# Optimization experiments

Measured on AMD Instinct MI355X. Metric: run time of the kernel, lower is better.

## Reference

```python
import jax, jax.numpy as jnp
import numpy as np

EMB = 1024
HEAD = 128

def setup_inputs() -> dict:
    key = jax.random.key(0)
    ks = jax.random.split(key, 7)
    B, S = 4, 4096
    x = jax.random.normal(ks[0], (B, S, EMB), dtype=jnp.float32)
    s_in = 1.0 / np.sqrt(EMB)
    Wq = jax.random.uniform(ks[1], (EMB, HEAD), jnp.float32, -s_in, s_in)
    bq = jax.random.uniform(ks[2], (HEAD,), jnp.float32, -s_in, s_in)
    Wk = jax.random.uniform(ks[3], (EMB, HEAD), jnp.float32, -s_in, s_in)
    bk = jax.random.uniform(ks[4], (HEAD,), jnp.float32, -s_in, s_in)
    Wv = jax.random.uniform(ks[5], (EMB, HEAD), jnp.float32, -s_in, s_in)
    bv = jax.random.uniform(ks[6], (HEAD,), jnp.float32, -s_in, s_in)
    return {"decoder_sequence": x, "Wq": Wq, "bq": bq, "Wk": Wk, "bk": bk, "Wv": Wv, "bv": bv}

def reference(decoder_sequence, Wq, bq, Wk, bk, Wv, bv):
    # QKV projections: [B,S,E] @ [E,H] -> [B,S,H]
    Q = decoder_sequence @ Wq + bq
    K = decoder_sequence @ Wk + bk
    V = decoder_sequence @ Wv + bv
    S = decoder_sequence.shape[1]
    scale = 1.0 / jnp.sqrt(jnp.asarray(HEAD, Q.dtype))
    # scores [B,S,S]
    A = jnp.einsum('bid,bjd->bij', Q, K) * scale
    causal = jnp.tril(jnp.ones((S, S), dtype=bool))  # keep lower-triangular incl. diag
    A = jnp.where(causal, A, -jnp.inf)
    A = jax.nn.softmax(A, axis=-1)
    return jnp.einsum('bij,bjd->bid', A, V)
```

## Files before the change

### kernel.cpp

```cpp
#include <hip/hip_runtime.h>
#include <hip/hip_bf16.h>
#include <math.h>

#define S_LEN 4096
#define EMB   1024
#define HEAD  128

typedef short bf16x8 __attribute__((ext_vector_type(8)));
typedef short s16x4  __attribute__((ext_vector_type(4)));
typedef float f32x4  __attribute__((ext_vector_type(4)));
typedef unsigned u32x2 __attribute__((ext_vector_type(2)));
typedef unsigned u32x4 __attribute__((ext_vector_type(4)));

static __device__ __forceinline__ short f2bf(float x){
  unsigned u = __builtin_bit_cast(unsigned, x);
  u += 0x7fffu + ((u >> 16) & 1u);
  return (short)(u >> 16);
}
static __device__ __forceinline__ float bf2f(short s){
  unsigned u = ((unsigned)(unsigned short)s) << 16;
  return __builtin_bit_cast(float, u);
}
static __device__ __forceinline__ unsigned cvtpk(float a, float b){
  unsigned r;
  asm("v_cvt_pk_bf16_f32 %0, %1, %2" : "=v"(r) : "v"(a), "v"(b));
  return r;
}
static __device__ __forceinline__ f32x4 mfma16(bf16x8 a, bf16x8 b, f32x4 c){
  return __builtin_amdgcn_mfma_f32_16x16x32_bf16(a, b, c, 0, 0, 0);
}
static __device__ __forceinline__ void gload16(const void* g, void* l){
  __builtin_amdgcn_global_load_lds((const __attribute__((address_space(1))) unsigned*)g,
                                   (__attribute__((address_space(3))) unsigned*)l, 16, 0, 0);
}

__global__ void prep_w(const float* __restrict__ Wq, const float* __restrict__ bq,
                       const float* __restrict__ Wk, const float* __restrict__ bk,
                       const float* __restrict__ Wv, const float* __restrict__ bv,
                       short* __restrict__ WT, float* __restrict__ bias){
  const float QS = 0.08838834764831845f * 1.4426950408889634f;
  int idx = blockIdx.x * 256 + threadIdx.x;
  int nc  = idx >> 10;
  int k   = idx & 1023;
  int mat = nc >> 7;
  int n   = nc & 127;
  const float* W = (mat == 0) ? Wq : (mat == 1) ? Wk : Wv;
  float s = (mat == 0) ? QS : 1.0f;
  WT[idx] = f2bf(W[k * HEAD + n] * s);
  if (idx < 384){
    int m2 = idx >> 7, n2 = idx & 127;
    const float* bsrc = (m2 == 0) ? bq : (m2 == 1) ? bk : bv;
    float s2 = (m2 == 0) ? QS : 1.0f;
    bias[idx] = bsrc[n2] * s2;
  }
}

__global__ __launch_bounds__(1024) void qkv_proj(const float* __restrict__ x,
    const short* __restrict__ WT, const float* __restrict__ bias,
    short* __restrict__ Qo, short* __restrict__ Ko, short* __restrict__ VTo){
  __shared__ __align__(16) short Sm[2][32768];

  const int tid = threadIdx.x;
  const int wave = tid >> 6, lane = tid & 63, lr = lane & 15, hg = lane >> 4;
  const int wrg = wave >> 3, cg = wave & 7, fbase = cg * 3;
  const int row0 = blockIdx.x * 64;

  const f32x4 zero = {0.f, 0.f, 0.f, 0.f};
  f32x4 acc[2][3];
  #pragma unroll
  for (int rf = 0; rf < 2; ++rf)
    #pragma unroll
    for (int f = 0; f < 3; ++f) acc[rf][f] = zero;

#define WL(buf) (&Sm[buf][0])
#define XL(buf) ((float*)&Sm[buf][24576])

#define QKV_STAGE(buf, k0)                                                         \
  {                                                                                \
    _Pragma("unroll")                                                              \
    for (int s = 0; s < 3; ++s){                                                   \
      int slot = s * 16 + wave;                                                    \
      int ff = slot >> 1, ks = slot & 1;                                           \
      gload16(WT + (size_t)(ff * 16 + lr) * 1024 + (k0) + ks * 32 + hg * 8,        \
              WL(buf) + slot * 512);                                               \
    }                                                                              \
    {                                                                              \
      int rr = wave * 4 + hg;                                                      \
      int cs = lr ^ (rr & 15);                                                     \
      gload16(x + (size_t)(row0 + rr) * 1024 + (k0) + cs * 4,                      \
              XL(buf) + wave * 256);                                               \
    }                                                                              \
  }

  QKV_STAGE(0, 0)

  int cur = 0;
  for (int t = 0; t < 16; ++t){
    if (t < 15){
      QKV_STAGE(cur ^ 1, (t + 1) * 64)
      asm volatile("s_waitcnt vmcnt(4)" ::: "memory");
    } else {
      asm volatile("s_waitcnt vmcnt(0)" ::: "memory");
    }
    __builtin_amdgcn_s_barrier();
    asm volatile("" ::: "memory");

    bf16x8 a[2][2];
    #pragma unroll
    for (int rf = 0; rf < 2; ++rf){
      const int xr = wrg * 32 + rf * 16 + lr;
      #pragma unroll
      for (int ks = 0; ks < 2; ++ks){
        int s0 = ks * 8 + hg * 2;
        f32x4 xa = *(const f32x4*)&XL(cur)[xr * 64 + ((s0 ^ lr) << 2)];
        f32x4 xb = *(const f32x4*)&XL(cur)[xr * 64 + (((s0 + 1) ^ lr) << 2)];
        u32x4 pk = { cvtpk(xa[0], xa[1]), cvtpk(xa[2], xa[3]),
                     cvtpk(xb[0], xb[1]), cvtpk(xb[2], xb[3]) };
        a[rf][ks] = __builtin_bit_cast(bf16x8, pk);
      }
    }
    __builtin_amdgcn_s_setprio(1);
    #pragma unroll
    for (int fi = 0; fi < 3; ++fi){
      #pragma unroll
      for (int ks = 0; ks < 2; ++ks){
        bf16x8 bfr = *(const bf16x8*)&WL(cur)[((fbase + fi) * 2 + ks) * 512 + lane * 8];
        acc[0][fi] = mfma16(a[0][ks], bfr, acc[0][fi]);
        acc[1][fi] = mfma16(a[1][ks], bfr, acc[1][fi]);
      }
    }
    __builtin_amdgcn_s_setprio(0);
    asm volatile("" ::: "memory");
    __builtin_amdgcn_s_barrier();
    cur ^= 1;
  }

  short* Vb = &Sm[0][0];
  #pragma unroll
  for (int rf = 0; rf < 2; ++rf){
    #pragma unroll
    for (int fi = 0; fi < 3; ++fi){
      int f = fbase + fi;
      float bb = bias[f * 16 + lr];
      int rloc = wrg * 32 + rf * 16 + hg * 4;
      if (f < 16){
        short* dst = (f < 8) ? Qo : Ko;
        int col = (f & 7) * 16 + lr;
        #pragma unroll
        for (int r = 0; r < 4; ++r)
          dst[(size_t)(row0 + rloc + r) * HEAD + col] = f2bf(acc[rf][fi][r] + bb);
      } else {
        int vcol = (f - 16) * 16 + lr;
        #pragma unroll
        for (int r = 0; r < 4; ++r)
          Vb[vcol * 72 + rloc + r] = f2bf(acc[rf][fi][r] + bb);
      }
    }
  }
  __syncthreads();
  {
    int vcol = tid >> 3, sq = tid & 7;
    bf16x8 v = *(const bf16x8*)&Vb[vcol * 72 + sq * 8];
    int bb2 = row0 >> 12, ss = row0 & 4095;
    *(bf16x8*)(VTo + ((size_t)(bb2 * HEAD + vcol)) * S_LEN + ss + sq * 8) = v;
  }
}

#define PPS 36

__global__ __launch_bounds__(256) void attn(const short* __restrict__ Q,
    const short* __restrict__ K, const short* __restrict__ VT,
    short* __restrict__ Opart, float* __restrict__ Dn){
  __shared__ __align__(16) short Kl[2][4096];
  __shared__ __align__(16) short Vl[2][4096];
  __shared__ __align__(16) short Pl[4][2][16 * PPS];

  const int tid = threadIdx.x;
  const int wave = tid >> 6, lane = tid & 63, lr = lane & 15, hg = lane >> 4;
  const int b = blockIdx.x;
  const int i = blockIdx.y;

  int t, c, ns;
  if (i < 120){
    int acc2 = 0; t = 0; c = 0;
    #pragma unroll
    for (int tt = 0; tt < 32; ++tt){
      int nf = (tt >> 2) + ((tt & 3) == 3);
      if (i >= acc2 && i < acc2 + nf){ t = tt; c = i - acc2; }
      acc2 += nf;
    }
    ns = 16;
  } else if (i < 128){ int k = i - 120; t = 4 * k + 2; c = k; ns = 12; }
  else if (i < 136)  { int k = i - 128; t = 4 * k + 1; c = k; ns = 8; }
  else               { int k = i - 136; t = 4 * k;     c = k; ns = 4; }

  const int qt0  = t * 128;
  const int kvlo = c << 9;

  const short* Qg = Q  + ((size_t)b * S_LEN + qt0 + wave * 32) * HEAD;
  const short* Kg = K  + (size_t)b * S_LEN * HEAD;
  const short* Vg = VT + (size_t)b * HEAD * S_LEN;

  bf16x8 qf[2][4];
  #pragma unroll
  for (int qs = 0; qs < 2; ++qs)
    #pragma unroll
    for (int sl = 0; sl < 4; ++sl)
      qf[qs][sl] = *(const bf16x8*)(Qg + (size_t)(qs * 16 + lr) * HEAD + sl * 32 + hg * 8);

#define ATTN_STAGE(buf, j0)                                                        \
  {                                                                                \
    _Pragma("unroll")                                                              \
    for (int q = 0; q < 2; ++q){                                                   \
      int s = wave * 2 + q;                                                        \
      gload16(Kg + (size_t)((j0) + (s >> 2) * 16 + lr) * HEAD + (s & 3) * 32 + hg * 8, \
              &Kl[buf][s * 512]);                                                  \
    }                                                                              \
    _Pragma("unroll")                                                              \
    for (int q = 0; q < 2; ++q){                                                   \
      int s = wave * 2 + q;                                                        \
      gload16(Vg + (size_t)(s * 16 + lr) * S_LEN + (j0) + hg * 8,                  \
              &Vl[buf][s * 512]);                                                  \
    }                                                                              \
  }

  ATTN_STAGE(0, kvlo)

  const f32x4 zero = {0.f, 0.f, 0.f, 0.f};
  f32x4 acc[8][2];
  #pragma unroll
  for (int f = 0; f < 8; ++f){ acc[f][0] = zero; acc[f][1] = zero; }
  float den[2] = {0.f, 0.f};

  int cur = 0;
  for (int st = 0; st < ns; ++st){
    const int j0 = kvlo + st * 32;
    if (st + 1 < ns){
      ATTN_STAGE(cur ^ 1, j0 + 32)
      asm volatile("s_waitcnt vmcnt(4)" ::: "memory");
    } else {
      asm volatile("s_waitcnt vmcnt(0)" ::: "memory");
    }
    __builtin_amdgcn_s_barrier();
    asm volatile("" ::: "memory");

    f32x4 sc[2][2];
    __builtin_amdgcn_s_setprio(1);
    #pragma unroll
    for (int kvs = 0; kvs < 2; ++kvs){
      sc[kvs][0] = zero; sc[kvs][1] = zero;
      #pragma unroll
      for (int sl = 0; sl < 4; ++sl){
        bf16x8 kf = *(const bf16x8*)&Kl[cur][(kvs * 4 + sl) * 512 + lane * 8];
        sc[kvs][0] = mfma16(kf, qf[0][sl], sc[kvs][0]);
        sc[kvs][1] = mfma16(kf, qf[1][sl], sc[kvs][1]);
      }
    }
    __builtin_amdgcn_s_setprio(0);

    if (j0 + 31 > qt0 + wave * 32){
      #pragma unroll
      for (int qs = 0; qs < 2; ++qs){
        int qr0 = qt0 + wave * 32 + qs * 16;
        #pragma unroll
        for (int kvs = 0; kvs < 2; ++kvs){
          int kv0 = j0 + kvs * 16 + hg * 4;
          #pragma unroll
          for (int r = 0; r < 4; ++r)
            if (kv0 + r > qr0 + lr) sc[kvs][qs][r] = -INFINITY;
        }
      }
    }

    s16x4 pb[2][2];
    #pragma unroll
    for (int qs = 0; qs < 2; ++qs){
      float p0[4], p1[4];
      #pragma unroll
      for (int r = 0; r < 4; ++r){
        p0[r] = __builtin_exp2f(sc[0][qs][r]);
        p1[r] = __builtin_exp2f(sc[1][qs][r]);
        den[qs] += p0[r] + p1[r];
      }
      u32x2 w0 = { cvtpk(p0[0], p0[1]), cvtpk(p0[2], p0[3]) };
      u32x2 w1 = { cvtpk(p1[0], p1[1]), cvtpk(p1[2], p1[3]) };
      pb[qs][0] = __builtin_bit_cast(s16x4, w0);
      pb[qs][1] = __builtin_bit_cast(s16x4, w1);
    }

    #pragma unroll
    for (int qs = 0; qs < 2; ++qs){
      short* Pw = &Pl[wave][qs][0];
      *(s16x4*)(&Pw[lr * PPS + hg * 4])      = pb[qs][0];
      *(s16x4*)(&Pw[lr * PPS + 16 + hg * 4]) = pb[qs][1];
    }
    bf16x8 vf[8];
    #pragma unroll
    for (int f = 0; f < 8; ++f)
      vf[f] = *(const bf16x8*)&Vl[cur][f * 512 + lane * 8];
    bf16x8 pf[2];
    #pragma unroll
    for (int qs = 0; qs < 2; ++qs)
      pf[qs] = *(const bf16x8*)(&Pl[wave][qs][lr * PPS + hg * 8]);

    __builtin_amdgcn_s_setprio(1);
    #pragma unroll
    for (int f = 0; f < 8; ++f){
      acc[f][0] = mfma16(vf[f], pf[0], acc[f][0]);
      acc[f][1] = mfma16(vf[f], pf[1], acc[f][1]);
    }
    __builtin_amdgcn_s_setprio(0);

    asm volatile("" ::: "memory");
    __builtin_amdgcn_s_barrier();
    cur ^= 1;
  }

  #pragma unroll
  for (int qs = 0; qs < 2; ++qs){
    den[qs] += __shfl_xor(den[qs], 16);
    den[qs] += __shfl_xor(den[qs], 32);
  }

  const int pidx = b * 144 + i;
  short* Op = Opart + (size_t)pidx * 16384;
  #pragma unroll
  for (int qs = 0; qs < 2; ++qs){
    const int rowblk = wave * 2 + qs;
    #pragma unroll
    for (int f = 0; f < 8; ++f){
      s16x4 ov;
      #pragma unroll
      for (int r = 0; r < 4; ++r) ov[r] = f2bf(acc[f][qs][r]);
      *(s16x4*)(Op + (rowblk * 16 + lr) * 128 + f * 16 + hg * 4) = ov;
    }
    if (hg == 0)
      Dn[pidx * 128 + rowblk * 16 + lr] = den[qs];
  }
}

__global__ __launch_bounds__(512) void combine(const short* __restrict__ Opart,
    const float* __restrict__ Dn, float* __restrict__ out){
  const int bx = blockIdx.x, b = blockIdx.y;
  const int t = bx >> 1, sub = bx & 1;
  const int row = threadIdx.x >> 3;
  const int cgp = threadIdx.x & 7;
  const int rI = sub * 64 + row;
  const int a = t >> 2, bb = t & 3;
  const int Ffull = a * (2 * a + bb - 1);
  const int nfull = a + (bb == 3);
  const int nc = a + 1;
  const int ipart = (bb == 2) ? 120 + a : (bb == 1) ? 128 + a : 136 + a;

  float L = 0.f;
  float o[16];
  #pragma unroll
  for (int e = 0; e < 16; ++e) o[e] = 0.f;
  for (int cc = 0; cc < nc; ++cc){
    int ii = (cc < nfull) ? Ffull + cc : ipart;
    int id = b * 144 + ii;
    L += Dn[id * 128 + rI];
    const short* op = Opart + (size_t)id * 16384 + rI * 128 + cgp * 16;
    bf16x8 v0 = *(const bf16x8*)(op);
    bf16x8 v1 = *(const bf16x8*)(op + 8);
    #pragma unroll
    for (int e = 0; e < 8; ++e){
      o[e]     += bf2f(v0[e]);
      o[8 + e] += bf2f(v1[e]);
    }
  }
  float inv = 1.f / L;
  float* dst = out + ((size_t)b * S_LEN + t * 128 + rI) * HEAD + cgp * 16;
  #pragma unroll
  for (int e4 = 0; e4 < 4; ++e4){
    float4 w4 = { o[e4*4]*inv, o[e4*4+1]*inv, o[e4*4+2]*inv, o[e4*4+3]*inv };
    *(float4*)(dst + e4 * 4) = w4;
  }
}

extern "C" void kernel_launch(void* const* d_in, const int* in_sizes, int n_in,
                              void* d_out, int out_size, void* d_ws, size_t ws_size,
                              hipStream_t stream){
  const float* x  = (const float*)d_in[0];
  const float* Wq = (const float*)d_in[1];
  const float* bq = (const float*)d_in[2];
  const float* Wk = (const float*)d_in[3];
  const float* bk = (const float*)d_in[4];
  const float* Wv = (const float*)d_in[5];
  const float* bv = (const float*)d_in[6];
  float* out = (float*)d_out;

  char* ws = (char*)d_ws;
  short* WT    = (short*)(ws);
  float* bias  = (float*)(ws + 786432);
  short* Qb    = (short*)(ws + (1u << 20));
  short* Kb    = (short*)(ws + (1u << 20) + 4194304u);
  short* VTb   = (short*)(ws + (1u << 20) + 8388608u);
  short* Opart = (short*)(ws + 13631488u);
  float* Dn    = (float*)(ws + 32505856u);

  prep_w<<<1536, 256, 0, stream>>>(Wq, bq, Wk, bk, Wv, bv, WT, bias);
  qkv_proj<<<256, 1024, 0, stream>>>(x, WT, bias, Qb, Kb, VTb);
  attn<<<dim3(4, 144), 256, 0, stream>>>(Qb, Kb, VTb, Opart, Dn);
  combine<<<dim3(64, 4), 512, 0, stream>>>(Opart, Dn, out);
}
```

Baseline: 89.91 us.

## Double KV tile per pipeline stage to 64 and reuse a single P buffer

Each attention loop iteration now handles 64 keys instead of 32, which halves the number of stages and the barriers and waitcnts that come with them. K/V LDS buffers double in size, and the V staging layout is split into two 32-key halves. The P scratch buffer is shared across the two query sub-blocks, which are processed one after the other within a stage. This raises LDS use and register pressure (16 V fragments live at once) and may lower occupancy. The causal mask now applies to a wider tile.

```diff
diff --git a/kernel.cpp b/kernel.cpp
--- a/kernel.cpp
+++ b/kernel.cpp
@@ -166,14 +166,14 @@
   }
 }
 
-#define PPS 36
+#define PPS 68
 
 __global__ __launch_bounds__(256) void attn(const short* __restrict__ Q,
     const short* __restrict__ K, const short* __restrict__ VT,
     short* __restrict__ Opart, float* __restrict__ Dn){
-  __shared__ __align__(16) short Kl[2][4096];
-  __shared__ __align__(16) short Vl[2][4096];
-  __shared__ __align__(16) short Pl[4][2][16 * PPS];
+  __shared__ __align__(16) short Kl[2][8192];
+  __shared__ __align__(16) short Vl[2][8192];
+  __shared__ __align__(16) short Pl[4][16 * PPS];
 
   const int tid = threadIdx.x;
   const int wave = tid >> 6, lane = tid & 63, lr = lane & 15, hg = lane >> 4;
@@ -189,10 +189,10 @@
       if (i >= acc2 && i < acc2 + nf){ t = tt; c = i - acc2; }
       acc2 += nf;
     }
-    ns = 16;
-  } else if (i < 128){ int k = i - 120; t = 4 * k + 2; c = k; ns = 12; }
-  else if (i < 136)  { int k = i - 128; t = 4 * k + 1; c = k; ns = 8; }
-  else               { int k = i - 136; t = 4 * k;     c = k; ns = 4; }
+    ns = 8;
+  } else if (i < 128){ int k = i - 120; t = 4 * k + 2; c = k; ns = 6; }
+  else if (i < 136)  { int k = i - 128; t = 4 * k + 1; c = k; ns = 4; }
+  else               { int k = i - 136; t = 4 * k;     c = k; ns = 2; }
 
   const int qt0  = t * 128;
   const int kvlo = c << 9;
@@ -211,15 +211,17 @@
 #define ATTN_STAGE(buf, j0)                                                        \
   {                                                                                \
     _Pragma("unroll")                                                              \
-    for (int q = 0; q < 2; ++q){                                                   \
-      int s = wave * 2 + q;                                                        \
+    for (int q = 0; q < 4; ++q){                                                   \
+      int s = wave * 4 + q;                                                        \
       gload16(Kg + (size_t)((j0) + (s >> 2) * 16 + lr) * HEAD + (s & 3) * 32 + hg * 8, \
               &Kl[buf][s * 512]);                                                  \
     }                                                                              \
     _Pragma("unroll")                                                              \
-    for (int q = 0; q < 2; ++q){                                                   \
-      int s = wave * 2 + q;                                                        \
-      gload16(Vg + (size_t)(s * 16 + lr) * S_LEN + (j0) + hg * 8,                  \
+    for (int q = 0; q < 4; ++q){                                                   \
+      int s = wave * 4 + q;                                                        \
+      int db = (s < 8) ? s : s - 8;                                                \
+      int ko = (s < 8) ? 0 : 32;                                                   \
+      gload16(Vg + (size_t)(db * 16 + lr) * S_LEN + (j0) + ko + hg * 8,            \
               &Vl[buf][s * 512]);                                                  \
     }                                                                              \
   }
@@ -231,23 +233,24 @@
   #pragma unroll
   for (int f = 0; f < 8; ++f){ acc[f][0] = zero; acc[f][1] = zero; }
   float den[2] = {0.f, 0.f};
+  short* Pw = &Pl[wave][0];
 
   int cur = 0;
   for (int st = 0; st < ns; ++st){
-    const int j0 = kvlo + st * 32;
+    const int j0 = kvlo + st * 64;
     if (st + 1 < ns){
-      ATTN_STAGE(cur ^ 1, j0 + 32)
-      asm volatile("s_waitcnt vmcnt(4)" ::: "memory");
+      ATTN_STAGE(cur ^ 1, j0 + 64)
+      asm volatile("s_waitcnt vmcnt(8)" ::: "memory");
     } else {
       asm volatile("s_waitcnt vmcnt(0)" ::: "memory");
     }
     __builtin_amdgcn_s_barrier();
     asm volatile("" ::: "memory");
 
-    f32x4 sc[2][2];
+    f32x4 sc[4][2];
     __builtin_amdgcn_s_setprio(1);
     #pragma unroll
-    for (int kvs = 0; kvs < 2; ++kvs){
+    for (int kvs = 0; kvs < 4; ++kvs){
       sc[kvs][0] = zero; sc[kvs][1] = zero;
       #pragma unroll
       for (int sl = 0; sl < 4; ++sl){
@@ -258,12 +261,12 @@
     }
     __builtin_amdgcn_s_setprio(0);
 
-    if (j0 + 31 > qt0 + wave * 32){
+    if (j0 + 63 > qt0 + wave * 32){
       #pragma unroll
       for (int qs = 0; qs < 2; ++qs){
         int qr0 = qt0 + wave * 32 + qs * 16;
         #pragma unroll
-        for (int kvs = 0; kvs < 2; ++kvs){
+        for (int kvs = 0; kvs < 4; ++kvs){
           int kv0 = j0 + kvs * 16 + hg * 4;
           #pragma unroll
           for (int r = 0; r < 4; ++r)
@@ -272,44 +275,40 @@
       }
     }
 
-    s16x4 pb[2][2];
+    bf16x8 vfa[8], vfb[8];
+    #pragma unroll
+    for (int f = 0; f < 8; ++f){
+      vfa[f] = *(const bf16x8*)&Vl[cur][f * 512 + lane * 8];
+      vfb[f] = *(const bf16x8*)&Vl[cur][(8 + f) * 512 + lane * 8];
+    }
+
     #pragma unroll
     for (int qs = 0; qs < 2; ++qs){
-      float p0[4], p1[4];
-      #pragma unroll
-      for (int r = 0; r < 4; ++r){
-        p0[r] = __builtin_exp2f(sc[0][qs][r]);
-        p1[r] = __builtin_exp2f(sc[1][qs][r]);
-        den[qs] += p0[r] + p1[r];
-      }
-      u32x2 w0 = { cvtpk(p0[0], p0[1]), cvtpk(p0[2], p0[3]) };
-      u32x2 w1 = { cvtpk(p1[0], p1[1]), cvtpk(p1[2], p1[3]) };
-      pb[qs][0] = __builtin_bit_cast(s16x4, w0);
-      pb[qs][1] = __builtin_bit_cast(s16x4, w1);
-    }
-
-    #pragma unroll
-    for (int qs = 0; qs < 2; ++qs){
-      short* Pw = &Pl[wave][qs][0];
-      *(s16x4*)(&Pw[lr * PPS + hg * 4])      = pb[qs][0];
-      *(s16x4*)(&Pw[lr * PPS + 16 + hg * 4]) = pb[qs][1];
-    }
-    bf16x8 vf[8];
-    #pragma unroll
-    for (int f = 0; f < 8; ++f)
-      vf[f] = *(const bf16x8*)&Vl[cur][f * 512 + lane * 8];
-    bf16x8 pf[2];
-    #pragma unroll
-    for (int qs = 0; qs < 2; ++qs)
-      pf[qs] = *(const bf16x8*)(&Pl[wave][qs][lr * PPS + hg * 8]);
-
-    __builtin_amdgcn_s_setprio(1);
-    #pragma unroll
-    for (int f = 0; f < 8; ++f){
-      acc[f][0] = mfma16(vf[f], pf[0], acc[f][0]);
-      acc[f][1] = mfma16(vf[f], pf[1], acc[f][1]);
-    }
-    __builtin_amdgcn_s_setprio(0);
+      float p[4][4];
+      #pragma unroll
+      for (int kvs = 0; kvs < 4; ++kvs){
+        #pragma unroll
+        for (int r = 0; r < 4; ++r){
+          p[kvs][r] = __builtin_exp2f(sc[kvs][qs][r]);
+          den[qs] += p[kvs][r];
+        }
+      }
+      #pragma unroll
+      for (int kvs = 0; kvs < 4; ++kvs){
+        u32x2 w = { cvtpk(p[kvs][0], p[kvs][1]), cvtpk(p[kvs][2], p[kvs][3]) };
+        *(u32x2*)(&Pw[lr * PPS + kvs * 16 + hg * 4]) = w;
+      }
+      bf16x8 pf0 = *(const bf16x8*)(&Pw[lr * PPS + hg * 8]);
+      bf16x8 pf1 = *(const bf16x8*)(&Pw[lr * PPS + 32 + hg * 8]);
+
+      __builtin_amdgcn_s_setprio(1);
+      #pragma unroll
+      for (int f = 0; f < 8; ++f){
+        acc[f][qs] = mfma16(vfa[f], pf0, acc[f][qs]);
+        acc[f][qs] = mfma16(vfb[f], pf1, acc[f][qs]);
+      }
+      __builtin_amdgcn_s_setprio(0);
+    }
 
     asm volatile("" ::: "memory");
     __builtin_amdgcn_s_barrier();
```

Result: slower. 106.3 us (+18.3%).
